# Optimization experiments

Measured on AMD Instinct MI355X. Metric: run time of the kernel, lower is better.

Reference implementation:

```python
import jax, jax.numpy as jnp
import numpy as np

N_NODES = 50000
N_EDGES = 800000
D_IN, D_HID, D_ENC = 256, 128, 64


def setup_inputs() -> dict:
    key = jax.random.key(0)
    ks = jax.random.split(key, 8)
    x = jax.random.normal(ks[0], (N_NODES, D_IN), dtype=jnp.float32)
    edge_index = jax.random.randint(ks[1], (2, N_EDGES), 0, N_NODES, dtype=jnp.int64)
    # GCNConv params: lin weight (no bias) + separate bias, stored as [in, out]
    W1 = jax.random.normal(ks[2], (D_IN, D_HID), dtype=jnp.float32) * (1.0 / np.sqrt(D_IN))
    b1 = jnp.zeros((D_HID,), dtype=jnp.float32)
    W2 = jax.random.normal(ks[3], (D_HID, D_ENC), dtype=jnp.float32) * (1.0 / np.sqrt(D_HID))
    b2 = jnp.zeros((D_ENC,), dtype=jnp.float32)
    Wfc = jax.random.normal(ks[4], (D_ENC, 1), dtype=jnp.float32) * (1.0 / np.sqrt(D_ENC))
    bfc = jnp.zeros((1,), dtype=jnp.float32)
    return {"x": x, "edge_index": edge_index, "W1": W1, "b1": b1,
            "W2": W2, "b2": b2, "Wfc": Wfc, "bfc": bfc}


def gcn_conv(x, W, b, row, col, norm, n_nodes):
    """PyG GCNConv (normalize=True): D^-1/2 (A+I) D^-1/2 X W + b."""
    h = x @ W                                   # [N, out]
    msg = h[row] * norm[:, None]                # [E+N, out] gather + scale
    out = jax.ops.segment_sum(msg, col, num_segments=n_nodes)  # scatter-add
    return out + b


def gcn_norm(edge_index, n_nodes, dtype):
    loop = jnp.arange(n_nodes, dtype=edge_index.dtype)
    row = jnp.concatenate([edge_index[0], loop])  # sources
    col = jnp.concatenate([edge_index[1], loop])  # targets
    deg = jax.ops.segment_sum(jnp.ones_like(col, dtype=dtype), col,
                              num_segments=n_nodes)
    dinv = jnp.where(deg > 0, jax.lax.rsqrt(jnp.maximum(deg, 1e-12)), 0.0)
    norm = dinv[row] * dinv[col]
    return row, col, norm


def reference(x, edge_index, W1, b1, W2, b2, Wfc, bfc):
    n = x.shape[0]
    row, col, norm = gcn_norm(edge_index, n, x.dtype)
    h = gcn_conv(x, W1, b1, row, col, norm, n)
    h = jax.nn.relu(h)
    # dropout p=0 / eval mode: identity
    h = gcn_conv(h, W2, b2, row, col, norm, n)
    out = jax.nn.sigmoid(h @ Wfc + bfc)          # [N, 1]
    return out
```

## Files before the change

### kernel.cpp

```cpp
#include <hip/hip_runtime.h>
#include <hip/hip_bf16.h>
#include <cmath>

#define N_NODES 50000
#define N_EDGES 800000
#define D_IN 256
#define D_HID 128
#define D_ENC 64
#define NBUK 128
#define BSH 9
#define BMSK 511
#define BCAP 16384
#define PB_EPT 16

typedef short short8 __attribute__((ext_vector_type(8)));
typedef float floatx4 __attribute__((ext_vector_type(4)));
typedef float floatx8 __attribute__((ext_vector_type(8)));
typedef unsigned short ushort8v __attribute__((ext_vector_type(8)));

static __device__ __forceinline__ unsigned short f2bf(float f) {
    unsigned int u = __float_as_uint(f);
    unsigned int r = (u + 0x7FFFu + ((u >> 16) & 1u)) >> 16;
    return (unsigned short)r;
}
static __device__ __forceinline__ float bf2f(unsigned short u) {
    return __uint_as_float(((unsigned int)u) << 16);
}
static __device__ __forceinline__ floatx8 bf2f8(ushort8v u) {
    floatx8 f;
#pragma unroll
    for (int j = 0; j < 8; ++j) f[j] = bf2f(u[j]);
    return f;
}

static __device__ __forceinline__ void wswz(const float* __restrict__ W,
                                            unsigned short* __restrict__ Wsw,
                                            int t, int K, int N) {
    int KS = K / 32;
    int lane = t & 63;
    int ks   = (t >> 6) % KS;
    int ct   = (t >> 6) / KS;
    int m = lane & 15, quad = lane >> 4;
    int kbase = ks * 32 + quad * 8;
    int col   = ct * 16 + m;
#pragma unroll
    for (int j = 0; j < 8; ++j)
        Wsw[t * 8 + j] = f2bf(W[(size_t)(kbase + j) * N + col]);
}

__global__ __launch_bounds__(256) void part_k(const int* __restrict__ rows,
                                              const int* __restrict__ cols,
                                              int* __restrict__ bcur,
                                              unsigned int* __restrict__ brecs,
                                              const float* __restrict__ W1,
                                              const float* __restrict__ W2,
                                              const float* __restrict__ b2,
                                              const float* __restrict__ Wfc,
                                              unsigned short* __restrict__ Wsw1,
                                              float* __restrict__ w2fc,
                                              float* __restrict__ b2fc) {
    __shared__ unsigned int recs[256 * PB_EPT];
    __shared__ int h[NBUK], ex[NBUK], gbase[NBUK];
    int tid = threadIdx.x;
    int t = blockIdx.x * 256 + tid;
    if (t < 4096) wswz(W1, Wsw1, t, D_IN, D_HID);
    else if (t < 4224) {
        int c = t - 4096;
        float s = 0.0f;
#pragma unroll 8
        for (int j = 0; j < D_ENC; ++j) s += W2[c * D_ENC + j] * Wfc[j];
        w2fc[c] = s;
    } else if (t == 4224) {
        float s = 0.0f;
        for (int j = 0; j < D_ENC; ++j) s += b2[j] * Wfc[j];
        b2fc[0] = s;
    }

    if (tid < NBUK) h[tid] = 0;
    __syncthreads();
    int e0 = blockIdx.x * (256 * PB_EPT);
    unsigned int myrec[PB_EPT];
    int myb[PB_EPT];
#pragma unroll
    for (int j = 0; j < PB_EPT; ++j) {
        int e = e0 + j * 256 + tid;
        if (e < N_EDGES) {
            int s = rows[e], d = cols[e];
            myrec[j] = ((unsigned int)s << 16) | (unsigned int)d;
            myb[j] = d >> BSH;
            atomicAdd(&h[myb[j]], 1);
        } else myb[j] = -1;
    }
    __syncthreads();
    if (tid < NBUK) {
        int c = h[tid];
        gbase[tid] = tid * BCAP + (c ? atomicAdd(&bcur[tid], c) : 0);
        ex[tid] = c;
    }
    __syncthreads();
    for (int off = 1; off < NBUK; off <<= 1) {
        int v = 0;
        if (tid < NBUK && tid >= off) v = ex[tid - off];
        __syncthreads();
        if (tid < NBUK) ex[tid] += v;
        __syncthreads();
    }
    if (tid < NBUK) { ex[tid] -= h[tid]; h[tid] = 0; }
    __syncthreads();
#pragma unroll
    for (int j = 0; j < PB_EPT; ++j) {
        if (myb[j] >= 0) {
            int p = ex[myb[j]] + atomicAdd(&h[myb[j]], 1);
            recs[p] = myrec[j];
        }
    }
    __syncthreads();
    int w = tid >> 6, lane = tid & 63;
    for (int b = w; b < NBUK; b += 4) {
        int start = ex[b], cnt = h[b], gb = gbase[b];
        int lim = (b + 1) * BCAP;
        for (int i = lane; i < cnt; i += 64) {
            int gp = gb + i;
            if (gp < lim) brecs[gp] = recs[start + i];
        }
    }
}

__global__ __launch_bounds__(512) void bucket_csr_k(const unsigned int* __restrict__ brecs,
                                                    const int* __restrict__ bcur,
                                                    int* __restrict__ rowptr,
                                                    int* __restrict__ rowcnt,
                                                    unsigned short* __restrict__ srcs,
                                                    float* __restrict__ dinv) {
    __shared__ int s[512];
    __shared__ int cur[512];
    __shared__ unsigned short sl[BCAP];
    int b = blockIdx.x;
    int cb = bcur[b]; if (cb > BCAP) cb = BCAP;
    int ebeg = b * BCAP, eend = ebeg + cb;
    int tid = threadIdx.x;
    s[tid] = 0;
    __syncthreads();
    for (int e = ebeg + tid; e < eend; e += 512)
        atomicAdd(&s[brecs[e] & BMSK], 1);
    __syncthreads();
    int v = s[tid];
    for (int off = 1; off < 512; off <<= 1) {
        int t = (tid >= off) ? s[tid - off] : 0;
        __syncthreads();
        s[tid] += t;
        __syncthreads();
    }
    int excl = s[tid] - v;
    cur[tid] = excl;
    int node = (b << BSH) + tid;
    if (node < N_NODES) {
        rowptr[node] = ebeg + excl;
        rowcnt[node] = v;
        dinv[node] = rsqrtf((float)(v + 1));
    }
    __syncthreads();
    for (int e = ebeg + tid; e < eend; e += 512) {
        unsigned int rec = brecs[e];
        int p = atomicAdd(&cur[rec & BMSK], 1);
        sl[p] = (unsigned short)(rec >> 16);
    }
    __syncthreads();
    int nw = (cb + 1) >> 1;
    unsigned int* s32 = (unsigned int*)(srcs + ebeg);
    const unsigned int* l32 = (const unsigned int*)sl;
    for (int t = tid; t < nw; t += 512) s32[t] = l32[t];
}

template<int K, int N, bool IN_BF16>
__global__ __launch_bounds__(256) void gemm_mfma_k(const void* __restrict__ Xv,
                                                   const unsigned short* __restrict__ Wsw,
                                                   const float* __restrict__ dinv,
                                                   unsigned short* __restrict__ H, int n) {
    constexpr int KS = K / 32, CT = N / 16, KP = K + 8;
    __shared__ unsigned short As[64 * KP];
    int row0 = blockIdx.x * 64;
    if (IN_BF16) {
        const ushort8v* X8 = (const ushort8v*)Xv;
        constexpr int NF8 = 64 * (K / 8);
        for (int idx = threadIdx.x; idx < NF8; idx += 256) {
            int r = idx / (K / 8), c8 = idx % (K / 8);
            int gr = row0 + r;
            ushort8v v = (gr < n) ? X8[(size_t)gr * (K / 8) + c8] : (ushort8v)0;
            *(ushort8v*)&As[r * KP + c8 * 8] = v;
        }
    } else {
        const float4* X4 = (const float4*)Xv;
        constexpr int NF4 = 64 * (K / 4);
        for (int idx = threadIdx.x; idx < NF4; idx += 256) {
            int r = idx / (K / 4), c4 = idx % (K / 4);
            int gr = row0 + r;
            float4 v = (gr < n) ? X4[(size_t)gr * (K / 4) + c4] : float4{0, 0, 0, 0};
            __hip_bfloat162 p0 = __float22bfloat162_rn(float2{v.x, v.y});
            __hip_bfloat162 p1 = __float22bfloat162_rn(float2{v.z, v.w});
            uint2 u; u.x = *(unsigned int*)&p0; u.y = *(unsigned int*)&p1;
            *(uint2*)&As[r * KP + c4 * 4] = u;
        }
    }
    __syncthreads();

    int w    = threadIdx.x >> 6;
    int lane = threadIdx.x & 63;
    int m    = lane & 15;
    int quad = lane >> 4;

    floatx4 acc[CT];
#pragma unroll
    for (int ct = 0; ct < CT; ++ct)
#pragma unroll
        for (int i = 0; i < 4; ++i) acc[ct][i] = 0.0f;

#pragma unroll
    for (int ks = 0; ks < KS; ++ks) {
        short8 af = *(const short8*)&As[(w * 16 + m) * KP + ks * 32 + quad * 8];
#pragma unroll
        for (int ct = 0; ct < CT; ++ct) {
            short8 bf = *(const short8*)&Wsw[(size_t)((ct * KS + ks) * 64 + lane) * 8];
            acc[ct] = __builtin_amdgcn_mfma_f32_16x16x32_bf16(af, bf, acc[ct], 0, 0, 0);
        }
    }

    int rbase = row0 + w * 16 + quad * 4;
    float dv[4];
#pragma unroll
    for (int reg = 0; reg < 4; ++reg) {
        int r = rbase + reg;
        dv[reg] = (r < n) ? dinv[r] : 0.0f;
    }
#pragma unroll
    for (int ct = 0; ct < CT; ++ct)
#pragma unroll
        for (int reg = 0; reg < 4; ++reg) {
            int r = rbase + reg;
            if (r < n) H[(size_t)r * N + ct * 16 + m] = f2bf(acc[ct][reg] * dv[reg]);
        }
}

#define GATHER_LOOP(SP, STRIDE, D)                                             \
    {                                                                          \
        const auto* sp_ = (SP);                                                \
        int i = 0;                                                             \
        for (; i + 8 <= cnt; i += 8) {                                         \
            int s0 = sp_[i],     s1 = sp_[i + 1], s2 = sp_[i + 2], s3 = sp_[i + 3]; \
            int s4 = sp_[i + 4], s5 = sp_[i + 5], s6 = sp_[i + 6], s7 = sp_[i + 7]; \
            ushort8v v0 = hs[(size_t)s0 * STRIDE + D], v1 = hs[(size_t)s1 * STRIDE + D]; \
            ushort8v v2 = hs[(size_t)s2 * STRIDE + D], v3 = hs[(size_t)s3 * STRIDE + D]; \
            ushort8v v4 = hs[(size_t)s4 * STRIDE + D], v5 = hs[(size_t)s5 * STRIDE + D]; \
            ushort8v v6 = hs[(size_t)s6 * STRIDE + D], v7 = hs[(size_t)s7 * STRIDE + D]; \
            a0 += bf2f8(v0); a1 += bf2f8(v1); a2 += bf2f8(v2); a3 += bf2f8(v3); \
            a0 += bf2f8(v4); a1 += bf2f8(v5); a2 += bf2f8(v6); a3 += bf2f8(v7); \
        }                                                                      \
        if (i + 4 <= cnt) {                                                    \
            int s0 = sp_[i], s1 = sp_[i + 1], s2 = sp_[i + 2], s3 = sp_[i + 3]; \
            a0 += bf2f8(hs[(size_t)s0 * STRIDE + D]);                          \
            a1 += bf2f8(hs[(size_t)s1 * STRIDE + D]);                          \
            a2 += bf2f8(hs[(size_t)s2 * STRIDE + D]);                          \
            a3 += bf2f8(hs[(size_t)s3 * STRIDE + D]);                          \
            i += 4;                                                            \
        }                                                                      \
        for (; i < cnt; ++i)                                                   \
            a0 += bf2f8(hs[(size_t)sp_[i] * STRIDE + D]);                      \
    }

__global__ __launch_bounds__(256) void g1z_k(const ushort8v* __restrict__ hs,
                                             const int* __restrict__ rowptr,
                                             const int* __restrict__ rowcnt,
                                             const unsigned short* __restrict__ srcs,
                                             const float* __restrict__ dinv,
                                             const float4* __restrict__ b1_4,
                                             const float4* __restrict__ w2fc4,
                                             float* __restrict__ z) {
    __shared__ unsigned short sidx[1024];
    __shared__ int sb2[2];
    int tid = threadIdx.x;
    int nodeb = blockIdx.x * 16;
    int ln = tid >> 4;
    int d8 = tid & 15;
    int node = nodeb + ln;
    int beg = rowptr[node];
    int cnt = rowcnt[node];
    if (tid == 0)   sb2[0] = beg;
    if (tid == 240) sb2[1] = beg + cnt;
    ushort8v selfv = hs[(size_t)node * 16 + d8];
    float di = dinv[node];
    __syncthreads();
    int base = sb2[0], total = sb2[1] - base;
    for (int t = tid; t < total && t < 1024; t += 256) sidx[t] = srcs[base + t];
    __syncthreads();

    floatx8 a0 = {0,0,0,0,0,0,0,0}, a1 = a0, a2 = a0, a3 = a0;
    if (total <= 1024) {
        GATHER_LOOP(sidx + (beg - base), 16, d8)
    } else {
        GATHER_LOOP(srcs + beg, 16, d8)
    }
    floatx8 acc = a0 + a1 + a2 + a3 + bf2f8(selfv);
    float4 bA = b1_4[d8 * 2],  bB = b1_4[d8 * 2 + 1];
    float4 wA = w2fc4[d8 * 2], wB = w2fc4[d8 * 2 + 1];
    float s = fmaxf(di * acc[0] + bA.x, 0.0f) * wA.x
            + fmaxf(di * acc[1] + bA.y, 0.0f) * wA.y
            + fmaxf(di * acc[2] + bA.z, 0.0f) * wA.z
            + fmaxf(di * acc[3] + bA.w, 0.0f) * wA.w
            + fmaxf(di * acc[4] + bB.x, 0.0f) * wB.x
            + fmaxf(di * acc[5] + bB.y, 0.0f) * wB.y
            + fmaxf(di * acc[6] + bB.z, 0.0f) * wB.z
            + fmaxf(di * acc[7] + bB.w, 0.0f) * wB.w;
#pragma unroll
    for (int off = 8; off; off >>= 1) s += __shfl_xor(s, off, 16);
    if (d8 == 0) z[node] = di * s;
}

__global__ __launch_bounds__(256) void gatherz_k(const float* __restrict__ z,
                                                 const int* __restrict__ rowptr,
                                                 const int* __restrict__ rowcnt,
                                                 const unsigned short* __restrict__ srcs,
                                                 const float* __restrict__ dinv,
                                                 const float* __restrict__ b2fc,
                                                 const float* __restrict__ bfc,
                                                 float* __restrict__ out) {
    int v = blockIdx.x * 256 + threadIdx.x;
    if (v >= N_NODES) return;
    int beg = rowptr[v], cnt = rowcnt[v];
    float s0 = z[v], s1 = 0.0f, s2 = 0.0f, s3 = 0.0f;
    int i = beg, end = beg + cnt;
    for (; i + 4 <= end; i += 4) {
        s0 += z[srcs[i]];
        s1 += z[srcs[i + 1]];
        s2 += z[srcs[i + 2]];
        s3 += z[srcs[i + 3]];
    }
    for (; i < end; ++i) s0 += z[srcs[i]];
    float p = dinv[v] * (s0 + s1 + s2 + s3) + b2fc[0] + bfc[0];
    out[v] = 1.0f / (1.0f + expf(-p));
}

extern "C" void kernel_launch(void* const* d_in, const int* in_sizes, int n_in,
                              void* d_out, int out_size, void* d_ws, size_t ws_size,
                              hipStream_t stream) {
    const float* x   = (const float*)d_in[0];
    const int*   ei  = (const int*)d_in[1];
    const float* W1  = (const float*)d_in[2];
    const float* b1  = (const float*)d_in[3];
    const float* W2  = (const float*)d_in[4];
    const float* b2  = (const float*)d_in[5];
    const float* Wfc = (const float*)d_in[6];
    const float* bfc = (const float*)d_in[7];
    float* out = (float*)d_out;

    const int* rows = ei;
    const int* cols = ei + N_EDGES;

    float* ws     = (float*)d_ws;
    float* dinv   = ws;
    int*   rowptr = (int*)(ws + 50048);
    int*   rowcnt = rowptr + 50048;
    int*   bcur   = rowcnt + 50048;
    unsigned int* brecs = (unsigned int*)(bcur + 128);
    unsigned short* srcs = (unsigned short*)(brecs + NBUK * BCAP);
    unsigned short* h1 = srcs + (size_t)NBUK * BCAP;
    unsigned short* Wsw1 = h1 + (size_t)N_NODES * D_HID;
    float* z    = (float*)(Wsw1 + (size_t)D_IN * D_HID);
    float* w2fc = z + 50000;
    float* b2fc = w2fc + 128;

    hipMemsetAsync(bcur, 0, NBUK * sizeof(int), stream);
    part_k<<<(N_EDGES + 256 * PB_EPT - 1) / (256 * PB_EPT), 256, 0, stream>>>(
        rows, cols, bcur, brecs, W1, W2, b2, Wfc, Wsw1, w2fc, b2fc);
    bucket_csr_k<<<(N_NODES + 511) / 512, 512, 0, stream>>>(brecs, bcur, rowptr, rowcnt, srcs, dinv);

    gemm_mfma_k<D_IN, D_HID, false><<<(N_NODES + 63) / 64, 256, 0, stream>>>(x, Wsw1, dinv, h1, N_NODES);

    g1z_k<<<N_NODES / 16, 256, 0, stream>>>((const ushort8v*)h1, rowptr, rowcnt, srcs, dinv,
                                            (const float4*)b1, (const float4*)w2fc, z);

    gatherz_k<<<(N_NODES + 255) / 256, 256, 0, stream>>>(z, rowptr, rowcnt, srcs, dinv,
                                                         b2fc, bfc, out);
}
```

Before: 179.3 us.

## Merge CSR build and first GEMM into one launch, move dinv scaling to gather

Result: faster. 164.9 us (-8.0%).

```diff
diff --git a/kernel.cpp b/kernel.cpp
--- a/kernel.cpp
+++ b/kernel.cpp
@@ -12,6 +12,8 @@
 #define BMSK 511
 #define BCAP 16384
 #define PB_EPT 16
+#define NCSRB 98
+#define NGEMB 782
 
 typedef short short8 __attribute__((ext_vector_type(8)));
 typedef float floatx4 __attribute__((ext_vector_type(4)));
@@ -126,145 +128,137 @@
     }
 }
 
-__global__ __launch_bounds__(512) void bucket_csr_k(const unsigned int* __restrict__ brecs,
-                                                    const int* __restrict__ bcur,
-                                                    int* __restrict__ rowptr,
-                                                    int* __restrict__ rowcnt,
-                                                    unsigned short* __restrict__ srcs,
-                                                    float* __restrict__ dinv) {
-    __shared__ int s[512];
-    __shared__ int cur[512];
-    __shared__ unsigned short sl[BCAP];
-    int b = blockIdx.x;
-    int cb = bcur[b]; if (cb > BCAP) cb = BCAP;
-    int ebeg = b * BCAP, eend = ebeg + cb;
+__global__ __launch_bounds__(512) void csr_gemm_k(const unsigned int* __restrict__ brecs,
+                                                  const int* __restrict__ bcur,
+                                                  int* __restrict__ rowptr,
+                                                  int* __restrict__ rowcnt,
+                                                  unsigned short* __restrict__ srcs,
+                                                  float* __restrict__ dinv,
+                                                  const float4* __restrict__ X4,
+                                                  const unsigned short* __restrict__ Wsw,
+                                                  unsigned short* __restrict__ H) {
+    extern __shared__ char dynsm[];
     int tid = threadIdx.x;
-    s[tid] = 0;
-    __syncthreads();
-    for (int e = ebeg + tid; e < eend; e += 512)
-        atomicAdd(&s[brecs[e] & BMSK], 1);
-    __syncthreads();
-    int v = s[tid];
-    for (int off = 1; off < 512; off <<= 1) {
-        int t = (tid >= off) ? s[tid - off] : 0;
-        __syncthreads();
-        s[tid] += t;
-        __syncthreads();
-    }
-    int excl = s[tid] - v;
-    cur[tid] = excl;
-    int node = (b << BSH) + tid;
-    if (node < N_NODES) {
-        rowptr[node] = ebeg + excl;
-        rowcnt[node] = v;
-        dinv[node] = rsqrtf((float)(v + 1));
-    }
-    __syncthreads();
-    for (int e = ebeg + tid; e < eend; e += 512) {
-        unsigned int rec = brecs[e];
-        int p = atomicAdd(&cur[rec & BMSK], 1);
-        sl[p] = (unsigned short)(rec >> 16);
-    }
-    __syncthreads();
-    int nw = (cb + 1) >> 1;
-    unsigned int* s32 = (unsigned int*)(srcs + ebeg);
-    const unsigned int* l32 = (const unsigned int*)sl;
-    for (int t = tid; t < nw; t += 512) s32[t] = l32[t];
-}
-
-template<int K, int N, bool IN_BF16>
-__global__ __launch_bounds__(256) void gemm_mfma_k(const void* __restrict__ Xv,
-                                                   const unsigned short* __restrict__ Wsw,
-                                                   const float* __restrict__ dinv,
-                                                   unsigned short* __restrict__ H, int n) {
-    constexpr int KS = K / 32, CT = N / 16, KP = K + 8;
-    __shared__ unsigned short As[64 * KP];
-    int row0 = blockIdx.x * 64;
-    if (IN_BF16) {
-        const ushort8v* X8 = (const ushort8v*)Xv;
-        constexpr int NF8 = 64 * (K / 8);
-        for (int idx = threadIdx.x; idx < NF8; idx += 256) {
-            int r = idx / (K / 8), c8 = idx % (K / 8);
+    if (blockIdx.x < NCSRB) {
+        int* s   = (int*)dynsm;
+        int* cur = (int*)(dynsm + 2048);
+        unsigned short* sl = (unsigned short*)(dynsm + 4096);
+        int b = blockIdx.x;
+        int cb = bcur[b]; if (cb > BCAP) cb = BCAP;
+        int ebeg = b * BCAP, eend = ebeg + cb;
+        s[tid] = 0;
+        __syncthreads();
+        for (int e = ebeg + tid; e < eend; e += 512)
+            atomicAdd(&s[brecs[e] & BMSK], 1);
+        __syncthreads();
+        int v = s[tid];
+        for (int off = 1; off < 512; off <<= 1) {
+            int t = (tid >= off) ? s[tid - off] : 0;
+            __syncthreads();
+            s[tid] += t;
+            __syncthreads();
+        }
+        int excl = s[tid] - v;
+        cur[tid] = excl;
+        int node = (b << BSH) + tid;
+        if (node < N_NODES) {
+            rowptr[node] = ebeg + excl;
+            rowcnt[node] = v;
+            dinv[node] = rsqrtf((float)(v + 1));
+        }
+        __syncthreads();
+        for (int e = ebeg + tid; e < eend; e += 512) {
+            unsigned int rec = brecs[e];
+            int p = atomicAdd(&cur[rec & BMSK], 1);
+            sl[p] = (unsigned short)(rec >> 16);
+        }
+        __syncthreads();
+        int nw = (cb + 1) >> 1;
+        unsigned int* s32 = (unsigned int*)(srcs + ebeg);
+        const unsigned int* l32 = (const unsigned int*)sl;
+        for (int t = tid; t < nw; t += 512) s32[t] = l32[t];
+    } else {
+        constexpr int KP = D_IN + 8;
+        unsigned short* As = (unsigned short*)dynsm;
+        int row0 = (blockIdx.x - NCSRB) * 64;
+        for (int idx = tid; idx < 64 * 64; idx += 512) {
+            int r = idx >> 6, c4 = idx & 63;
             int gr = row0 + r;
-            ushort8v v = (gr < n) ? X8[(size_t)gr * (K / 8) + c8] : (ushort8v)0;
-            *(ushort8v*)&As[r * KP + c8 * 8] = v;
-        }
-    } else {
-        const float4* X4 = (const float4*)Xv;
-        constexpr int NF4 = 64 * (K / 4);
-        for (int idx = threadIdx.x; idx < NF4; idx += 256) {
-            int r = idx / (K / 4), c4 = idx % (K / 4);
-            int gr = row0 + r;
-            float4 v = (gr < n) ? X4[(size_t)gr * (K / 4) + c4] : float4{0, 0, 0, 0};
+            float4 v = (gr < N_NODES) ? X4[(size_t)gr * 64 + c4] : float4{0, 0, 0, 0};
             __hip_bfloat162 p0 = __float22bfloat162_rn(float2{v.x, v.y});
             __hip_bfloat162 p1 = __float22bfloat162_rn(float2{v.z, v.w});
             uint2 u; u.x = *(unsigned int*)&p0; u.y = *(unsigned int*)&p1;
             *(uint2*)&As[r * KP + c4 * 4] = u;
         }
-    }
-    __syncthreads();
-
-    int w    = threadIdx.x >> 6;
-    int lane = threadIdx.x & 63;
-    int m    = lane & 15;
-    int quad = lane >> 4;
-
-    floatx4 acc[CT];
-#pragma unroll
-    for (int ct = 0; ct < CT; ++ct)
-#pragma unroll
-        for (int i = 0; i < 4; ++i) acc[ct][i] = 0.0f;
-
-#pragma unroll
-    for (int ks = 0; ks < KS; ++ks) {
-        short8 af = *(const short8*)&As[(w * 16 + m) * KP + ks * 32 + quad * 8];
-#pragma unroll
-        for (int ct = 0; ct < CT; ++ct) {
-            short8 bf = *(const short8*)&Wsw[(size_t)((ct * KS + ks) * 64 + lane) * 8];
-            acc[ct] = __builtin_amdgcn_mfma_f32_16x16x32_bf16(af, bf, acc[ct], 0, 0, 0);
-        }
-    }
-
-    int rbase = row0 + w * 16 + quad * 4;
-    float dv[4];
-#pragma unroll
-    for (int reg = 0; reg < 4; ++reg) {
-        int r = rbase + reg;
-        dv[reg] = (r < n) ? dinv[r] : 0.0f;
-    }
-#pragma unroll
-    for (int ct = 0; ct < CT; ++ct)
-#pragma unroll
-        for (int reg = 0; reg < 4; ++reg) {
-            int r = rbase + reg;
-            if (r < n) H[(size_t)r * N + ct * 16 + m] = f2bf(acc[ct][reg] * dv[reg]);
-        }
-}
-
-#define GATHER_LOOP(SP, STRIDE, D)                                             \
+        __syncthreads();
+
+        int w    = tid >> 6;
+        int lane = tid & 63;
+        int m    = lane & 15;
+        int quad = lane >> 4;
+        int rsub = w & 3;
+        int cth  = w >> 2;
+
+        floatx4 acc[4];
+#pragma unroll
+        for (int ct = 0; ct < 4; ++ct)
+#pragma unroll
+            for (int i = 0; i < 4; ++i) acc[ct][i] = 0.0f;
+
+#pragma unroll
+        for (int ks = 0; ks < D_IN / 32; ++ks) {
+            short8 af = *(const short8*)&As[(rsub * 16 + m) * KP + ks * 32 + quad * 8];
+#pragma unroll
+            for (int ct = 0; ct < 4; ++ct) {
+                int ct4 = cth * 4 + ct;
+                short8 bf = *(const short8*)&Wsw[(size_t)((ct4 * (D_IN / 32) + ks) * 64 + lane) * 8];
+                acc[ct] = __builtin_amdgcn_mfma_f32_16x16x32_bf16(af, bf, acc[ct], 0, 0, 0);
+            }
+        }
+
+        int rbase = row0 + rsub * 16 + quad * 4;
+#pragma unroll
+        for (int ct = 0; ct < 4; ++ct) {
+            int col = (cth * 4 + ct) * 16 + m;
+#pragma unroll
+            for (int reg = 0; reg < 4; ++reg) {
+                int r = rbase + reg;
+                if (r < N_NODES) H[(size_t)r * D_HID + col] = f2bf(acc[ct][reg]);
+            }
+        }
+    }
+}
+
+#define WGATHER(SP)                                                            \
     {                                                                          \
         const auto* sp_ = (SP);                                                \
         int i = 0;                                                             \
         for (; i + 8 <= cnt; i += 8) {                                         \
             int s0 = sp_[i],     s1 = sp_[i + 1], s2 = sp_[i + 2], s3 = sp_[i + 3]; \
             int s4 = sp_[i + 4], s5 = sp_[i + 5], s6 = sp_[i + 6], s7 = sp_[i + 7]; \
-            ushort8v v0 = hs[(size_t)s0 * STRIDE + D], v1 = hs[(size_t)s1 * STRIDE + D]; \
-            ushort8v v2 = hs[(size_t)s2 * STRIDE + D], v3 = hs[(size_t)s3 * STRIDE + D]; \
-            ushort8v v4 = hs[(size_t)s4 * STRIDE + D], v5 = hs[(size_t)s5 * STRIDE + D]; \
-            ushort8v v6 = hs[(size_t)s6 * STRIDE + D], v7 = hs[(size_t)s7 * STRIDE + D]; \
-            a0 += bf2f8(v0); a1 += bf2f8(v1); a2 += bf2f8(v2); a3 += bf2f8(v3); \
-            a0 += bf2f8(v4); a1 += bf2f8(v5); a2 += bf2f8(v6); a3 += bf2f8(v7); \
+            float w0 = dinv[s0], w1 = dinv[s1], w2 = dinv[s2], w3 = dinv[s3];  \
+            float w4 = dinv[s4], w5 = dinv[s5], w6 = dinv[s6], w7 = dinv[s7];  \
+            ushort8v v0 = hs[(size_t)s0 * 16 + d8], v1 = hs[(size_t)s1 * 16 + d8]; \
+            ushort8v v2 = hs[(size_t)s2 * 16 + d8], v3 = hs[(size_t)s3 * 16 + d8]; \
+            ushort8v v4 = hs[(size_t)s4 * 16 + d8], v5 = hs[(size_t)s5 * 16 + d8]; \
+            ushort8v v6 = hs[(size_t)s6 * 16 + d8], v7 = hs[(size_t)s7 * 16 + d8]; \
+            a0 += bf2f8(v0) * w0; a1 += bf2f8(v1) * w1;                        \
+            a2 += bf2f8(v2) * w2; a3 += bf2f8(v3) * w3;                        \
+            a0 += bf2f8(v4) * w4; a1 += bf2f8(v5) * w5;                        \
+            a2 += bf2f8(v6) * w6; a3 += bf2f8(v7) * w7;                        \
         }                                                                      \
         if (i + 4 <= cnt) {                                                    \
             int s0 = sp_[i], s1 = sp_[i + 1], s2 = sp_[i + 2], s3 = sp_[i + 3]; \
-            a0 += bf2f8(hs[(size_t)s0 * STRIDE + D]);                          \
-            a1 += bf2f8(hs[(size_t)s1 * STRIDE + D]);                          \
-            a2 += bf2f8(hs[(size_t)s2 * STRIDE + D]);                          \
-            a3 += bf2f8(hs[(size_t)s3 * STRIDE + D]);                          \
+            a0 += bf2f8(hs[(size_t)s0 * 16 + d8]) * dinv[s0];                  \
+            a1 += bf2f8(hs[(size_t)s1 * 16 + d8]) * dinv[s1];                  \
+            a2 += bf2f8(hs[(size_t)s2 * 16 + d8]) * dinv[s2];                  \
+            a3 += bf2f8(hs[(size_t)s3 * 16 + d8]) * dinv[s3];                  \
             i += 4;                                                            \
         }                                                                      \
-        for (; i < cnt; ++i)                                                   \
-            a0 += bf2f8(hs[(size_t)sp_[i] * STRIDE + D]);                      \
+        for (; i < cnt; ++i) {                                                 \
+            int s = sp_[i];                                                    \
+            a0 += bf2f8(hs[(size_t)s * 16 + d8]) * dinv[s];                    \
+        }                                                                      \
     }
 
 __global__ __launch_bounds__(256) void g1z_k(const ushort8v* __restrict__ hs,
@@ -295,11 +289,11 @@
 
     floatx8 a0 = {0,0,0,0,0,0,0,0}, a1 = a0, a2 = a0, a3 = a0;
     if (total <= 1024) {
-        GATHER_LOOP(sidx + (beg - base), 16, d8)
+        WGATHER(sidx + (beg - base))
     } else {
-        GATHER_LOOP(srcs + beg, 16, d8)
-    }
-    floatx8 acc = a0 + a1 + a2 + a3 + bf2f8(selfv);
+        WGATHER(srcs + beg)
+    }
+    floatx8 acc = a0 + a1 + a2 + a3 + bf2f8(selfv) * di;
     float4 bA = b1_4[d8 * 2],  bB = b1_4[d8 * 2 + 1];
     float4 wA = w2fc4[d8 * 2], wB = w2fc4[d8 * 2 + 1];
     float s = fmaxf(di * acc[0] + bA.x, 0.0f) * wA.x
@@ -371,9 +365,9 @@
     hipMemsetAsync(bcur, 0, NBUK * sizeof(int), stream);
     part_k<<<(N_EDGES + 256 * PB_EPT - 1) / (256 * PB_EPT), 256, 0, stream>>>(
         rows, cols, bcur, brecs, W1, W2, b2, Wfc, Wsw1, w2fc, b2fc);
-    bucket_csr_k<<<(N_NODES + 511) / 512, 512, 0, stream>>>(brecs, bcur, rowptr, rowcnt, srcs, dinv);
-
-    gemm_mfma_k<D_IN, D_HID, false><<<(N_NODES + 63) / 64, 256, 0, stream>>>(x, Wsw1, dinv, h1, N_NODES);
+
+    csr_gemm_k<<<NCSRB + NGEMB, 512, 36864, stream>>>(brecs, bcur, rowptr, rowcnt, srcs, dinv,
+                                                      (const float4*)x, Wsw1, h1);
 
     g1z_k<<<N_NODES / 16, 256, 0, stream>>>((const ushort8v*)h1, rowptr, rowcnt, srcs, dinv,
                                             (const float4*)b1, (const float4*)w2fc, z);
```
